# Performance work log

Measured on AMD Instinct MI355X. Metric: run time of the kernel, lower is better.

The kernel has to match this reference:

```python
import jax, jax.numpy as jnp
import numpy as np

B, S, E = 2, 2048, 2048
H, D = 16, 128  # num_heads, head_dim; H*D == E
EPS = 1e-5


def setup_inputs() -> dict:
    key = jax.random.key(0)
    ks = jax.random.split(key, 9)
    s = 0.02
    return {
        "x": jax.random.normal(ks[0], (B, S, E), dtype=jnp.float32),
        "ln1_scale": jnp.ones((E,), dtype=jnp.float32),
        "Wq": jax.random.normal(ks[1], (E, H, D), dtype=jnp.float32) * s,
        "Wk": jax.random.normal(ks[2], (E, H, D), dtype=jnp.float32) * s,
        "Wv": jax.random.normal(ks[3], (E, H, D), dtype=jnp.float32) * s,
        "Wo": jax.random.normal(ks[4], (H, D, E), dtype=jnp.float32) * s,
        "ln2_scale": jnp.ones((E,), dtype=jnp.float32),
        "Wmlp": jax.random.normal(ks[5], (E, E), dtype=jnp.float32) * s,
        "bmlp": jnp.zeros((E,), dtype=jnp.float32),
    }


def _rmsnorm(x, scale, eps=EPS):
    var = jnp.mean(jnp.square(x), axis=-1, keepdims=True)
    return x * jax.lax.rsqrt(var + eps) * scale


def _causal_mha(x, Wq, Wk, Wv, Wo):
    # x: [B,S,E] -> q,k,v: [B,S,H,D]
    q = jnp.einsum("bse,ehd->bshd", x, Wq)
    k = jnp.einsum("bse,ehd->bshd", x, Wk)
    v = jnp.einsum("bse,ehd->bshd", x, Wv)
    scale = 1.0 / jnp.sqrt(jnp.float32(q.shape[-1]))
    scores = jnp.einsum("bqhd,bkhd->bhqk", q, k) * scale  # [B,H,S,S]
    causal = jnp.tril(jnp.ones((x.shape[1], x.shape[1]), dtype=bool))
    scores = jnp.where(causal[None, None], scores, jnp.finfo(scores.dtype).min)
    probs = jax.nn.softmax(scores, axis=-1)
    ctx = jnp.einsum("bhqk,bkhd->bqhd", probs, v)  # [B,S,H,D]
    return jnp.einsum("bqhd,hde->bqe", ctx, Wo)


def reference(x, ln1_scale, Wq, Wk, Wv, Wo, ln2_scale, Wmlp, bmlp):
    # TinyLlamaBlock, schedule[layer_id] == ANCHOR (full causal MHA), use_rope=False
    normed = _rmsnorm(x, ln1_scale)
    attn_out = _causal_mha(normed, Wq, Wk, Wv, Wo)
    x = x + attn_out
    x = x + (_rmsnorm(x, ln2_scale) @ Wmlp + bmlp)
    return x
```

## Files before the change

### kernel.cpp

```cpp
#include <hip/hip_runtime.h>


typedef unsigned short ushort_t;
typedef __attribute__((ext_vector_type(8))) short short8;
typedef __attribute__((ext_vector_type(4))) float floatx4;

__device__ __forceinline__ ushort_t f2bf(float f) {
  union { float f; unsigned u; } v; v.f = f;
  unsigned r = v.u + 0x7fffu + ((v.u >> 16) & 1u);
  return (ushort_t)(r >> 16);
}
__device__ __forceinline__ float bf2f(unsigned h) {
  union { unsigned u; float f; } v; v.u = h << 16; return v.f;
}
__device__ __forceinline__ void load16(const ushort_t* g, ushort_t* l) {
  __builtin_amdgcn_global_load_lds(
      (const __attribute__((address_space(1))) unsigned*)g,
      (__attribute__((address_space(3))) unsigned*)l, 16, 0, 0);
}

__global__ __launch_bounds__(256) void transpose_w_batch(
    const float* __restrict__ s0, const float* __restrict__ s1,
    const float* __restrict__ s2, ushort_t* __restrict__ d0,
    ushort_t* __restrict__ d1, ushort_t* __restrict__ d2) {
  __shared__ __align__(16) ushort_t tile[64][72];
  const float* src = s0;
  ushort_t* dst = d0;
  if (blockIdx.z == 1) { src = s1; dst = d1; }
  else if (blockIdx.z == 2) { src = s2; dst = d2; }
  const int t = threadIdx.x;
  const int n0 = blockIdx.x * 64, k0 = blockIdx.y * 64;
#pragma unroll
  for (int i = 0; i < 4; ++i) {
    int c = t + 256 * i;
    int r = c >> 4, o = (c & 15) * 4;
    float4 raw = *(const float4*)&src[(size_t)(k0 + r) * 2048 + n0 + o];
    tile[o + 0][r] = f2bf(raw.x);
    tile[o + 1][r] = f2bf(raw.y);
    tile[o + 2][r] = f2bf(raw.z);
    tile[o + 3][r] = f2bf(raw.w);
  }
  __syncthreads();
#pragma unroll
  for (int i = 0; i < 2; ++i) {
    int c = t + 256 * i;
    int r = c >> 3, o = (c & 7) * 8;
    *(uint4*)&dst[(size_t)(n0 + r) * 2048 + k0 + o] = *(const uint4*)&tile[r][o];
  }
}

template <bool XBF>
__global__ __launch_bounds__(256) void rmsnorm_kernel(
    const void* __restrict__ xv, int in_ld, const float* __restrict__ g,
    ushort_t* __restrict__ out, int out_ld) {
  const int row = blockIdx.x, t = threadIdx.x;
  float v[8];
  if (XBF) {
    uint4 raw = *(const uint4*)((const ushort_t*)xv + (size_t)row * in_ld + t * 8);
    v[0] = bf2f(raw.x & 0xffffu); v[1] = bf2f(raw.x >> 16);
    v[2] = bf2f(raw.y & 0xffffu); v[3] = bf2f(raw.y >> 16);
    v[4] = bf2f(raw.z & 0xffffu); v[5] = bf2f(raw.z >> 16);
    v[6] = bf2f(raw.w & 0xffffu); v[7] = bf2f(raw.w >> 16);
  } else {
    const float* xr = (const float*)xv + (size_t)row * in_ld + t * 8;
    float4 a = *(const float4*)xr;
    float4 b = *(const float4*)(xr + 4);
    v[0] = a.x; v[1] = a.y; v[2] = a.z; v[3] = a.w;
    v[4] = b.x; v[5] = b.y; v[6] = b.z; v[7] = b.w;
  }
  float ss = 0.f;
#pragma unroll
  for (int i = 0; i < 8; ++i) ss += v[i] * v[i];
#pragma unroll
  for (int m = 32; m >= 1; m >>= 1) ss += __shfl_xor(ss, m, 64);
  __shared__ float red[4];
  if ((t & 63) == 0) red[t >> 6] = ss;
  __syncthreads();
  float rs = rsqrtf((red[0] + red[1] + red[2] + red[3]) * (1.0f / 2048.0f) + 1e-5f);
  const float* gp = g + t * 8;
  float4 ga = *(const float4*)gp;
  float4 gb = *(const float4*)(gp + 4);
  float gv[8] = {ga.x, ga.y, ga.z, ga.w, gb.x, gb.y, gb.z, gb.w};
  union { ushort_t u16[8]; uint4 u; } p;
#pragma unroll
  for (int i = 0; i < 8; ++i) p.u16[i] = f2bf(v[i] * rs * gv[i]);
  *(uint4*)&out[(size_t)row * out_ld + t * 8] = p.u;
}

template <int MODE>
__global__ __launch_bounds__(256, 2) void gemm_bt(
    const ushort_t* A, int lda, const ushort_t* Bt, const ushort_t* Bt2,
    int ldb, void* Cv, int ldc, const void* resid, int ldr,
    const float* bias, int M, int N, int K) {
  __shared__ __align__(16) ushort_t As[128][64];
  __shared__ __align__(16) ushort_t Bs[128][64];
  const int t = threadIdx.x;
  const int wid = t >> 6, lane = t & 63;
  const int l15 = lane & 15, quad = lane >> 4;
  const int m0 = blockIdx.y * 128, n0 = blockIdx.x * 128;
  const int wm = (wid >> 1) * 64, wn = (wid & 1) * 64;

  const ushort_t* btb = Bt;
  int nr = n0;
  if (Bt2 != nullptr && n0 >= 4096) { btb = Bt2; nr = n0 - 4096; }

  const int srow = wid * 8 + (lane >> 3);
  const int scol = ((lane & 7) ^ ((lane >> 3) & 7)) * 8;
  const ushort_t* ag = &A[(size_t)(m0 + srow) * lda + scol];
  const ushort_t* bg = &btb[(size_t)(nr + srow) * ldb + scol];
  ushort_t* al = &As[wid * 8][0];
  ushort_t* bl = &Bs[wid * 8][0];

  floatx4 acc[4][4];
#pragma unroll
  for (int i = 0; i < 4; ++i)
#pragma unroll
    for (int j = 0; j < 4; ++j) acc[i][j] = (floatx4){0.f, 0.f, 0.f, 0.f};

  const char* asb = (const char*)&As[0][0];
  const char* bsb = (const char*)&Bs[0][0];
  const int rswz = (l15 & 7);

  for (int k0 = 0; k0 < K; k0 += 64) {
    __syncthreads();
#pragma unroll
    for (int s = 0; s < 4; ++s) {
      load16(ag + (size_t)(s * 32) * lda + k0, al + s * 32 * 64);
      load16(bg + (size_t)(s * 32) * ldb + k0, bl + s * 32 * 64);
    }
    __syncthreads();

#pragma unroll
    for (int kh = 0; kh < 2; ++kh) {
      const int gsel = ((kh * 4 + quad) ^ rswz) * 16;
      short8 af[4], bf[4];
#pragma unroll
      for (int i = 0; i < 4; ++i)
        af[i] = *(const short8*)(asb + (wm + i * 16 + l15) * 128 + gsel);
#pragma unroll
      for (int j = 0; j < 4; ++j)
        bf[j] = *(const short8*)(bsb + (wn + j * 16 + l15) * 128 + gsel);
#pragma unroll
      for (int i = 0; i < 4; ++i)
#pragma unroll
        for (int j = 0; j < 4; ++j)
          acc[i][j] = __builtin_amdgcn_mfma_f32_16x16x32_bf16(af[i], bf[j],
                                                              acc[i][j], 0, 0, 0);
    }
  }

#pragma unroll
  for (int i = 0; i < 4; ++i)
#pragma unroll
    for (int j = 0; j < 4; ++j)
#pragma unroll
      for (int r = 0; r < 4; ++r) {
        int row = m0 + wm + i * 16 + quad * 4 + r;
        int col = n0 + wn + j * 16 + l15;
        float v = acc[i][j][r];
        if (MODE == 0) {
          ((ushort_t*)Cv)[(size_t)row * ldc + col] = f2bf(v);
        } else if (MODE == 1) {
          float rv = ((const float*)resid)[(size_t)row * ldr + col];
          ((ushort_t*)Cv)[(size_t)row * ldc + col] = f2bf(rv + v);
        } else {
          float rv = bf2f(((const ushort_t*)resid)[(size_t)row * ldr + col]);
          ((float*)Cv)[(size_t)row * ldc + col] = rv + v + bias[col];
        }
      }
}

__global__ __launch_bounds__(256) void transpose_v_kernel(
    const ushort_t* __restrict__ qkv, ushort_t* __restrict__ vT) {
  __shared__ __align__(16) ushort_t tile[64][72];
  const int t = threadIdx.x;
  const int s0 = blockIdx.x * 64, d0 = blockIdx.y * 64;
  const int bh = blockIdx.z, b = bh >> 4, h = bh & 15;
#pragma unroll
  for (int i = 0; i < 2; ++i) {
    int c = t + 256 * i, r = c >> 3, o = (c & 7) * 8;
    uint4 raw = *(const uint4*)&qkv[(size_t)(b * 2048 + s0 + r) * 6144 + 4096 +
                                    h * 128 + d0 + o];
    tile[o + 0][r] = (ushort_t)(raw.x & 0xffffu);
    tile[o + 1][r] = (ushort_t)(raw.x >> 16);
    tile[o + 2][r] = (ushort_t)(raw.y & 0xffffu);
    tile[o + 3][r] = (ushort_t)(raw.y >> 16);
    tile[o + 4][r] = (ushort_t)(raw.z & 0xffffu);
    tile[o + 5][r] = (ushort_t)(raw.z >> 16);
    tile[o + 6][r] = (ushort_t)(raw.w & 0xffffu);
    tile[o + 7][r] = (ushort_t)(raw.w >> 16);
  }
  __syncthreads();
#pragma unroll
  for (int i = 0; i < 2; ++i) {
    int c = t + 256 * i, r = c >> 3, o = (c & 7) * 8;
    *(uint4*)&vT[((size_t)bh * 128 + d0 + r) * 2048 + s0 + o] =
        *(const uint4*)&tile[r][o];
  }
}

__global__ __launch_bounds__(256, 2) void attn_kernel(
    const ushort_t* qkv, const ushort_t* vT, ushort_t* ctx, int ldctx) {
  const int S = 2048, LD = 6144, D = 128;
  __shared__ __align__(16) ushort_t Ks[2][64][136];
  __shared__ __align__(16) ushort_t Vt[2][128][72];
  __shared__ __align__(16) ushort_t Ps[4][16][72];
  const int t = threadIdx.x;
  const int wid = t >> 6, lane = t & 63;
  const int l15 = lane & 15, quad = lane >> 4;
  const int bx = (int)blockIdx.x;
  const int bh = blockIdx.y, b = bh >> 4, h = bh & 15;

  const int krow = t >> 4, kcol = (t & 15) * 8;
  const int vrow = t >> 3, vcol = (t & 7) * 8;
  const ushort_t* kgp = &qkv[(size_t)(b * S + krow) * LD + 2048 + h * D + kcol];
  const ushort_t* vgp = &vT[((size_t)bh * D + vrow) * S + vcol];

  uint4 k0r, k1r, k2r, k3r, v0r, v1r, v2r, v3r;
#define PREFETCH(KB)                                          \
  do {                                                        \
    const ushort_t* kp_ = kgp + (size_t)(KB)*LD;              \
    k0r = *(const uint4*)(kp_);                               \
    k1r = *(const uint4*)(kp_ + (size_t)16 * LD);             \
    k2r = *(const uint4*)(kp_ + (size_t)32 * LD);             \
    k3r = *(const uint4*)(kp_ + (size_t)48 * LD);             \
    const ushort_t* vp_ = vgp + (KB);                         \
    v0r = *(const uint4*)(vp_);                               \
    v1r = *(const uint4*)(vp_ + (size_t)32 * S);              \
    v2r = *(const uint4*)(vp_ + (size_t)64 * S);              \
    v3r = *(const uint4*)(vp_ + (size_t)96 * S);              \
  } while (0)
#define STAGE(BUF)                                            \
  do {                                                        \
    *(uint4*)&Ks[BUF][krow + 0][kcol]  = k0r;                 \
    *(uint4*)&Ks[BUF][krow + 16][kcol] = k1r;                 \
    *(uint4*)&Ks[BUF][krow + 32][kcol] = k2r;                 \
    *(uint4*)&Ks[BUF][krow + 48][kcol] = k3r;                 \
    *(uint4*)&Vt[BUF][vrow + 0][vcol]  = v0r;                 \
    *(uint4*)&Vt[BUF][vrow + 32][vcol] = v1r;                 \
    *(uint4*)&Vt[BUF][vrow + 64][vcol] = v2r;                 \
    *(uint4*)&Vt[BUF][vrow + 96][vcol] = v3r;                 \
  } while (0)

  const float sc2 = 0.08838834764831845f * 1.4426950408889634f;
  const int nkt0 = 32 - bx;
  const int NT = 33;

  PREFETCH(0);
  STAGE(0);
  PREFETCH(64);

  int g = 0;
  for (int ph = 0; ph < 2; ++ph) {
    const int qtile = ph == 0 ? (31 - bx) : bx;
    const int qb = qtile * 64;

    short8 qf[4];
    {
      const ushort_t* qp =
          &qkv[(size_t)(b * S + qb + wid * 16 + l15) * LD + h * D];
#pragma unroll
      for (int kk = 0; kk < 4; ++kk)
        qf[kk] = *(const short8*)&qp[kk * 32 + quad * 8];
    }

    floatx4 accO[8];
#pragma unroll
    for (int i = 0; i < 8; ++i) accO[i] = (floatx4){0.f, 0.f, 0.f, 0.f};
    float m_i = -1e30f;
    float l_i = 0.f;
    const int qg = qb + wid * 16 + l15;

    const int nkt = qtile + 1;
    for (int kt = 0; kt < nkt; ++kt, ++g) {
      const int kb = kt * 64;
      const int buf = g & 1;
      __syncthreads();
      if (g + 1 < NT) {
        STAGE(buf ^ 1);
        if (g + 2 < NT) {
          const int g2 = g + 2;
          const int kb2 = (g2 < nkt0) ? g2 * 64 : (g2 - nkt0) * 64;
          PREFETCH(kb2);
        }
      }

      floatx4 st[4];
#pragma unroll
      for (int jn = 0; jn < 4; ++jn) {
        st[jn] = (floatx4){0.f, 0.f, 0.f, 0.f};
#pragma unroll
        for (int kk = 0; kk < 4; ++kk) {
          short8 kf = *(const short8*)&Ks[buf][jn * 16 + l15][kk * 32 + quad * 8];
          st[jn] = __builtin_amdgcn_mfma_f32_16x16x32_bf16(kf, qf[kk], st[jn], 0, 0, 0);
        }
      }

      float p[4][4];
      if (kt == nkt - 1) {
#pragma unroll
        for (int jn = 0; jn < 4; ++jn)
#pragma unroll
          for (int r = 0; r < 4; ++r) {
            int kg = kb + jn * 16 + quad * 4 + r;
            float s = st[jn][r] * sc2;
            p[jn][r] = (kg <= qg) ? s : -1e30f;
          }
      } else {
#pragma unroll
        for (int jn = 0; jn < 4; ++jn)
#pragma unroll
          for (int r = 0; r < 4; ++r) p[jn][r] = st[jn][r] * sc2;
      }

      float mq0 = fmaxf(fmaxf(p[0][0], p[0][1]), fmaxf(p[0][2], p[0][3]));
      float mq1 = fmaxf(fmaxf(p[1][0], p[1][1]), fmaxf(p[1][2], p[1][3]));
      float mq2 = fmaxf(fmaxf(p[2][0], p[2][1]), fmaxf(p[2][2], p[2][3]));
      float mq3 = fmaxf(fmaxf(p[3][0], p[3][1]), fmaxf(p[3][2], p[3][3]));
      float v = fmaxf(fmaxf(mq0, mq1), fmaxf(mq2, mq3));
      v = fmaxf(v, __shfl_xor(v, 16, 64));
      v = fmaxf(v, __shfl_xor(v, 32, 64));

      if (!__all(v - m_i <= 8.0f)) {
        float mnew = fmaxf(m_i, v);
        float alpha = exp2f(m_i - mnew);
        m_i = mnew;
        float arow[4];
#pragma unroll
        for (int r = 0; r < 4; ++r) arow[r] = __shfl(alpha, quad * 4 + r, 16);
#pragma unroll
        for (int jd = 0; jd < 8; ++jd)
#pragma unroll
          for (int r = 0; r < 4; ++r) accO[jd][r] *= arow[r];
        l_i *= alpha;
      }

#pragma unroll
      for (int jn = 0; jn < 4; ++jn)
#pragma unroll
        for (int r = 0; r < 4; ++r) p[jn][r] = exp2f(p[jn][r] - m_i);

#pragma unroll
      for (int jn = 0; jn < 4; ++jn) {
        unsigned w0, w1;
        asm("v_cvt_pk_bf16_f32 %0, %1, %2" : "=v"(w0)
            : "v"(p[jn][0]), "v"(p[jn][1]));
        asm("v_cvt_pk_bf16_f32 %0, %1, %2" : "=v"(w1)
            : "v"(p[jn][2]), "v"(p[jn][3]));
        uint2 pk2; pk2.x = w0; pk2.y = w1;
        *(uint2*)&Ps[wid][l15][jn * 16 + quad * 4] = pk2;
      }

      float sq = ((p[0][0] + p[0][1]) + (p[0][2] + p[0][3])) +
                 ((p[1][0] + p[1][1]) + (p[1][2] + p[1][3])) +
                 ((p[2][0] + p[2][1]) + (p[2][2] + p[2][3])) +
                 ((p[3][0] + p[3][1]) + (p[3][2] + p[3][3]));
      sq += __shfl_xor(sq, 16, 64);
      sq += __shfl_xor(sq, 32, 64);
      l_i += sq;

      __asm__ __volatile__("s_waitcnt lgkmcnt(0)" ::: "memory");

      short8 pf[2];
#pragma unroll
      for (int kk = 0; kk < 2; ++kk)
        pf[kk] = *(const short8*)&Ps[wid][l15][kk * 32 + quad * 8];
#pragma unroll
      for (int jd = 0; jd < 8; ++jd)
#pragma unroll
        for (int kk = 0; kk < 2; ++kk) {
          short8 vf = *(const short8*)&Vt[buf][jd * 16 + l15][kk * 32 + quad * 8];
          accO[jd] = __builtin_amdgcn_mfma_f32_16x16x32_bf16(pf[kk], vf, accO[jd], 0, 0, 0);
        }
    }

    float lrow[4];
#pragma unroll
    for (int r = 0; r < 4; ++r) lrow[r] = 1.0f / __shfl(l_i, quad * 4 + r, 16);
#pragma unroll
    for (int jd = 0; jd < 8; ++jd)
#pragma unroll
      for (int r = 0; r < 4; ++r) {
        int row = b * S + qb + wid * 16 + quad * 4 + r;
        int col = h * D + jd * 16 + l15;
        ctx[(size_t)row * ldctx + col] = f2bf(accO[jd][r] * lrow[r]);
      }
  }
#undef PREFETCH
#undef STAGE
}

extern "C" void kernel_launch(void* const* d_in, const int* in_sizes, int n_in,
                              void* d_out, int out_size, void* d_ws,
                              size_t ws_size, hipStream_t stream) {
  const float* x    = (const float*)d_in[0];
  const float* ln1  = (const float*)d_in[1];
  const float* Wq   = (const float*)d_in[2];
  const float* Wk   = (const float*)d_in[3];
  const float* Wv   = (const float*)d_in[4];
  const float* Wo   = (const float*)d_in[5];
  const float* ln2  = (const float*)d_in[6];
  const float* Wmlp = (const float*)d_in[7];
  const float* bmlp = (const float*)d_in[8];
  float* out = (float*)d_out;

  char* ws = (char*)d_ws;
  ushort_t* qkv = (ushort_t*)(ws + 0);
  ushort_t* R2  = (ushort_t*)(ws + 50331648);
  ushort_t* WqT   = R2;
  ushort_t* WkT   = R2 + 4194304;
  ushort_t* WoT   = R2;
  ushort_t* WmlpT = R2 + 4194304;
  ushort_t* n1  = (ushort_t*)d_out;
  ushort_t* WvT = (ushort_t*)d_out + 8388608;
  ushort_t* vT  = (ushort_t*)d_out + 8388608;
  ushort_t* ctx = qkv + 4096;
  ushort_t* x1  = qkv + 2048;
  ushort_t* n2  = qkv;

  dim3 blk(256);
  dim3 ggrid(16, 32);
  dim3 ggridQKV(48, 32);

  rmsnorm_kernel<false><<<dim3(4096), blk, 0, stream>>>(x, 2048, ln1, n1, 2048);

  transpose_w_batch<<<dim3(32, 32, 3), blk, 0, stream>>>(Wq, Wk, Wv,
                                                         WqT, WkT, WvT);
  gemm_bt<0><<<ggridQKV, blk, 0, stream>>>(n1, 2048, WqT, WvT, 2048, qkv, 6144,
                                           nullptr, 0, nullptr, 4096, 6144, 2048);

  transpose_w_batch<<<dim3(32, 32, 2), blk, 0, stream>>>(Wo, Wmlp, Wo,
                                                         WoT, WmlpT, WoT);

  transpose_v_kernel<<<dim3(32, 2, 32), blk, 0, stream>>>(qkv, vT);

  attn_kernel<<<dim3(16, 32), blk, 0, stream>>>(qkv, vT, ctx, 6144);

  gemm_bt<1><<<ggrid, blk, 0, stream>>>(ctx, 6144, WoT, nullptr, 2048, x1, 6144,
                                        x, 2048, nullptr, 4096, 2048, 2048);

  rmsnorm_kernel<true><<<dim3(4096), blk, 0, stream>>>(x1, 6144, ln2, n2, 6144);

  gemm_bt<2><<<ggrid, blk, 0, stream>>>(n2, 6144, WmlpT, nullptr, 2048, out, 2048,
                                        x1, 6144, bmlp, 4096, 2048, 2048);
}
```

Before: 463.5 us.

## Double-buffer LDS tiles in bf16 GEMM to overlap global loads with MFMA

Converts the GEMM main loop from single-buffered load-then-compute into a two-stage pipeline. It prefetches tile k+2 into the freed LDS buffer while computing on the other, using explicit vmcnt waits, barriers, and sched_barriers. It also raises wave priority around the MFMA block. This doubles LDS use to 64KB per block, which may limit occupancy at the requested 2 blocks per CU.

```diff
diff --git a/kernel.cpp b/kernel.cpp
--- a/kernel.cpp
+++ b/kernel.cpp
@@ -92,8 +92,8 @@
     const ushort_t* A, int lda, const ushort_t* Bt, const ushort_t* Bt2,
     int ldb, void* Cv, int ldc, const void* resid, int ldr,
     const float* bias, int M, int N, int K) {
-  __shared__ __align__(16) ushort_t As[128][64];
-  __shared__ __align__(16) ushort_t Bs[128][64];
+  __shared__ __align__(16) ushort_t As[2][128][64];
+  __shared__ __align__(16) ushort_t Bs[2][128][64];
   const int t = threadIdx.x;
   const int wid = t >> 6, lane = t & 63;
   const int l15 = lane & 15, quad = lane >> 4;
@@ -108,8 +108,21 @@
   const int scol = ((lane & 7) ^ ((lane >> 3) & 7)) * 8;
   const ushort_t* ag = &A[(size_t)(m0 + srow) * lda + scol];
   const ushort_t* bg = &btb[(size_t)(nr + srow) * ldb + scol];
-  ushort_t* al = &As[wid * 8][0];
-  ushort_t* bl = &Bs[wid * 8][0];
+
+#define STAGE(BUF, TILE)                                                    \
+  do {                                                                      \
+    ushort_t* al_ = &As[BUF][wid * 8][0];                                   \
+    ushort_t* bl_ = &Bs[BUF][wid * 8][0];                                   \
+    const size_t ko_ = (size_t)(TILE)*64;                                   \
+    load16(ag + (size_t)0 * lda + ko_,   al_ + 0 * 32 * 64);                \
+    load16(ag + (size_t)32 * lda + ko_,  al_ + 1 * 32 * 64);                \
+    load16(ag + (size_t)64 * lda + ko_,  al_ + 2 * 32 * 64);                \
+    load16(ag + (size_t)96 * lda + ko_,  al_ + 3 * 32 * 64);                \
+    load16(bg + (size_t)0 * ldb + ko_,   bl_ + 0 * 32 * 64);                \
+    load16(bg + (size_t)32 * ldb + ko_,  bl_ + 1 * 32 * 64);                \
+    load16(bg + (size_t)64 * ldb + ko_,  bl_ + 2 * 32 * 64);                \
+    load16(bg + (size_t)96 * ldb + ko_,  bl_ + 3 * 32 * 64);                \
+  } while (0)
 
   floatx4 acc[4][4];
 #pragma unroll
@@ -117,19 +130,21 @@
 #pragma unroll
     for (int j = 0; j < 4; ++j) acc[i][j] = (floatx4){0.f, 0.f, 0.f, 0.f};
 
-  const char* asb = (const char*)&As[0][0];
-  const char* bsb = (const char*)&Bs[0][0];
   const int rswz = (l15 & 7);
-
-  for (int k0 = 0; k0 < K; k0 += 64) {
-    __syncthreads();
-#pragma unroll
-    for (int s = 0; s < 4; ++s) {
-      load16(ag + (size_t)(s * 32) * lda + k0, al + s * 32 * 64);
-      load16(bg + (size_t)(s * 32) * ldb + k0, bl + s * 32 * 64);
-    }
-    __syncthreads();
-
+  const int nt = K >> 6;
+
+  STAGE(0, 0);
+  STAGE(1, 1);
+  __asm__ __volatile__("s_waitcnt vmcnt(8)");
+  __builtin_amdgcn_sched_barrier(0);
+  __builtin_amdgcn_s_barrier();
+  __builtin_amdgcn_sched_barrier(0);
+
+  for (int tt = 0; tt < nt; ++tt) {
+    const int buf = tt & 1;
+    const char* asb = (const char*)&As[buf][0][0];
+    const char* bsb = (const char*)&Bs[buf][0][0];
+    __builtin_amdgcn_s_setprio(1);
 #pragma unroll
     for (int kh = 0; kh < 2; ++kh) {
       const int gsel = ((kh * 4 + quad) ^ rswz) * 16;
@@ -147,7 +162,23 @@
           acc[i][j] = __builtin_amdgcn_mfma_f32_16x16x32_bf16(af[i], bf[j],
                                                               acc[i][j], 0, 0, 0);
     }
-  }
+    __builtin_amdgcn_s_setprio(0);
+
+    if (tt + 1 < nt) {
+      __builtin_amdgcn_s_barrier();
+      __builtin_amdgcn_sched_barrier(0);
+      if (tt + 2 < nt) {
+        STAGE(buf, tt + 2);
+        __asm__ __volatile__("s_waitcnt vmcnt(8)");
+      } else {
+        __asm__ __volatile__("s_waitcnt vmcnt(0)");
+      }
+      __builtin_amdgcn_sched_barrier(0);
+      __builtin_amdgcn_s_barrier();
+      __builtin_amdgcn_sched_barrier(0);
+    }
+  }
+#undef STAGE
 
 #pragma unroll
   for (int i = 0; i < 4; ++i)
```

Result: faster. 453.8 us (-2.1%).
